# Kernel tuning notes

Measured on AMD Instinct MI355X. Metric: run time of the kernel, lower is better.

Reference implementation:

```python
import jax, jax.numpy as jnp
import numpy as np

B, N, M = 4, 8192, 8192

def setup_inputs() -> dict:
    key = jax.random.key(0)
    k1, k2 = jax.random.split(key)
    xyz1 = jax.random.normal(k1, (B, N, 3), dtype=jnp.float32)
    xyz2 = jax.random.normal(k2, (B, M, 3), dtype=jnp.float32)
    return {"xyz1": xyz1, "xyz2": xyz2}

def reference(xyz1, xyz2):
    sq1 = jnp.sum(xyz1 * xyz1, axis=-1)                      # [B,N]
    sq2 = jnp.sum(xyz2 * xyz2, axis=-1)                      # [B,M]
    inner = jnp.einsum('bnd,bmd->bnm', xyz1, xyz2)           # [B,N,M]
    d = sq1[:, :, None] + sq2[:, None, :] - 2.0 * inner      # squared dists
    dist1 = jnp.min(d, axis=2)                               # [B,N] nearest in xyz2
    dist2 = jnp.min(d, axis=1)                               # [B,M] nearest in xyz1
    return (dist1, dist2)
```

## Files before the change

kernel.cpp:

```cpp
#include <hip/hip_runtime.h>


typedef short bf16x8 __attribute__((ext_vector_type(8)));
typedef float f32x16 __attribute__((ext_vector_type(16)));

constexpr int Bc  = 4;
constexpr int Nc  = 8192;
constexpr int NT  = Nc / 32;
constexpr int SEG = 8;
constexpr int TPS = NT / SEG;

__device__ inline unsigned short f2bf(float x) {
    unsigned u = __float_as_uint(x);
    unsigned r = (u + 0x7FFFu + ((u >> 16) & 1u)) >> 16;
    return (unsigned short)r;
}
__device__ inline float bf2f(unsigned short h) {
    return __uint_as_float(((unsigned)h) << 16);
}
__device__ inline unsigned pack2(unsigned short lo, unsigned short hi) {
    return (unsigned)lo | ((unsigned)hi << 16);
}

__global__ void init_out_inf(float* __restrict__ out, int n) {
    int i = blockIdx.x * blockDim.x + threadIdx.x;
    int stride = gridDim.x * blockDim.x;
    for (; i < n; i += stride) out[i] = __uint_as_float(0x7F800000u);
}

__global__ void pack_both(const float* __restrict__ xyz1,
                          const float* __restrict__ xyz2,
                          uint4* __restrict__ qf, uint4* __restrict__ tf) {
    const int tid   = blockIdx.x * 256 + threadIdx.x;
    const int cloud = blockIdx.y;
    const float* src = cloud ? xyz2 : xyz1;
    const int lane = tid & 63;
    const int tile = (tid >> 6) & (NT - 1);
    const int b    = tid >> 14;
    const int pt   = tile * 32 + (lane & 31);
    const int kg   = lane >> 5;
    const float* p = src + ((size_t)b * Nc + pt) * 3;
    float x = p[0], y = p[1], z = p[2];
    float sq = x * x + y * y + z * z;
    unsigned short xh = f2bf(x), yh = f2bf(y), zh = f2bf(z);
    unsigned short xl = f2bf(x - bf2f(xh)), yl = f2bf(y - bf2f(yh)), zl = f2bf(z - bf2f(zh));
    unsigned short sh = f2bf(sq), sl = f2bf(sq - bf2f(sh));
    unsigned short m2xh = f2bf(-2.0f * bf2f(xh));
    unsigned short m2yh = f2bf(-2.0f * bf2f(yh));
    unsigned short m2zh = f2bf(-2.0f * bf2f(zh));
    unsigned short m2xl = f2bf(-2.0f * (x - bf2f(xh)));
    unsigned short m2yl = f2bf(-2.0f * (y - bf2f(yh)));
    unsigned short m2zl = f2bf(-2.0f * (z - bf2f(zh)));
    const unsigned short ONE = 0x3F80;
    uint4 q, t;
    if (kg == 0) {
        q.x = pack2(xh, xh); q.y = pack2(xl, yh);
        q.z = pack2(yh, yl); q.w = pack2(zh, zh);
        t.x = pack2(m2xh, m2xl); t.y = pack2(m2xh, m2yh);
        t.z = pack2(m2yl, m2yh); t.w = pack2(m2zh, m2zl);
    } else {
        q.x = pack2(zl, sh); q.y = pack2(sl, ONE);
        q.z = pack2(ONE, 0); q.w = 0;
        t.x = pack2(m2zh, ONE); t.y = pack2(ONE, sh);
        t.z = pack2(sl, 0);     t.w = 0;
    }
    const size_t FR = (size_t)Bc * NT * 64;
    qf[(size_t)cloud * FR + tid] = q;
    tf[(size_t)cloud * FR + tid] = t;
}

__global__ __launch_bounds__(256) void chamfer_dir(
    const uint4* __restrict__ qf,
    const uint4* __restrict__ tf,
    float* __restrict__ out) {
    __shared__ float sRed[4][32][33];
    const int tid = threadIdx.x, lane = tid & 63, wave = tid >> 6;
    const int z = blockIdx.z, dir = z >> 2, b = z & 3, seg = blockIdx.y;
    const int qc = dir, tc = dir ^ 1;
    const size_t FR = (size_t)Bc * NT * 64;

    const int n_tile = blockIdx.x * 4 + wave;
    const bf16x8 av = __builtin_bit_cast(bf16x8,
        qf[(size_t)qc * FR + ((size_t)(b * NT + n_tile)) * 64 + lane]);
    f32x16 zc{};
    float rmin[16];
    #pragma unroll
    for (int r = 0; r < 16; ++r) rmin[r] = INFINITY;

    const uint4* bp = tf + (size_t)tc * FR + ((size_t)(b * NT + seg * TPS)) * 64 + lane;
    #pragma unroll 4
    for (int mt = 0; mt < TPS; ++mt) {
        const bf16x8 bv = __builtin_bit_cast(bf16x8, bp[(size_t)mt * 64]);
        const f32x16 d = __builtin_amdgcn_mfma_f32_32x32x16_bf16(av, bv, zc, 0, 0, 0);
        #pragma unroll
        for (int r = 0; r < 16; ++r) rmin[r] = fminf(rmin[r], d[r]);
    }

    const int col = lane & 31, hi = lane >> 5;
    #pragma unroll
    for (int r = 0; r < 16; ++r) {
        const int row = (r & 3) + 8 * (r >> 2) + 4 * hi;
        sRed[wave][row][col] = rmin[r];
    }
    __syncthreads();

    const int row2 = tid >> 1, half = tid & 1;
    const int w = row2 >> 5, rr = row2 & 31;
    const float* rp = &sRed[w][rr][half * 16];
    float v0 = fminf(fminf(rp[0], rp[1]),  fminf(rp[2], rp[3]));
    float v1 = fminf(fminf(rp[4], rp[5]),  fminf(rp[6], rp[7]));
    float v2 = fminf(fminf(rp[8], rp[9]),  fminf(rp[10], rp[11]));
    float v3 = fminf(fminf(rp[12], rp[13]), fminf(rp[14], rp[15]));
    float v = fminf(fminf(v0, v1), fminf(v2, v3));
    v = fminf(v, __shfl_xor(v, 1));
    if (!half) {
        const int n = (blockIdx.x * 4 + w) * 32 + rr;
        unsigned* o = (unsigned*)out + (size_t)dir * Bc * Nc + (size_t)b * Nc + n;
        atomicMin(o, __float_as_uint(fmaxf(v, 0.0f)));
    }
}

constexpr int QPT = 2, TPB = 256;
__global__ void pack_pts(const float* __restrict__ src, float4* __restrict__ dst, int npts) {
    int i = blockIdx.x * blockDim.x + threadIdx.x;
    if (i < npts) {
        float x = src[3 * i], y = src[3 * i + 1], z = src[3 * i + 2];
        dst[i] = make_float4(x, y, z, x * x + y * y + z * z);
    }
}
__global__ __launch_bounds__(TPB, 8) void chamfer_fb(
    const float* __restrict__ xyz1, const float* __restrict__ xyz2,
    const float4* __restrict__ p1, const float4* __restrict__ p2,
    float* __restrict__ out) {
    const int z = blockIdx.z, dir = z >> 2, b = z & 3, seg = blockIdx.y;
    const float*  qry  = dir ? xyz2 : xyz1;
    const float4* tgt4 = dir ? p1 : p2;
    float* o = out + (size_t)dir * Bc * Nc + (size_t)b * Nc;
    const int q0 = blockIdx.x * (TPB * QPT) + threadIdx.x;
    float m2x[QPT], m2y[QPT], m2z[QPT], qsq[QPT];
    #pragma unroll
    for (int j = 0; j < QPT; ++j) {
        const float* qp = qry + ((size_t)b * Nc + q0 + j * TPB) * 3;
        float x = qp[0], y = qp[1], zz = qp[2];
        m2x[j] = -2.f * x; m2y[j] = -2.f * y; m2z[j] = -2.f * zz;
        qsq[j] = x * x + y * y + zz * zz;
    }
    constexpr int seg_pts = Nc / 16;
    const float4* t = tgt4 + (size_t)b * Nc + (size_t)seg * seg_pts;
    float mn0[QPT], mn1[QPT];
    #pragma unroll
    for (int j = 0; j < QPT; ++j) { mn0[j] = INFINITY; mn1[j] = INFINITY; }
    #pragma unroll 4
    for (int i = 0; i < seg_pts; i += 2) {
        const float4 t0 = t[i], t1 = t[i + 1];
        #pragma unroll
        for (int j = 0; j < QPT; ++j) {
            mn0[j] = fminf(mn0[j], fmaf(m2x[j], t0.x, fmaf(m2y[j], t0.y, fmaf(m2z[j], t0.z, t0.w))));
            mn1[j] = fminf(mn1[j], fmaf(m2x[j], t1.x, fmaf(m2y[j], t1.y, fmaf(m2z[j], t1.z, t1.w))));
        }
    }
    #pragma unroll
    for (int j = 0; j < QPT; ++j) {
        float d = fmaxf(qsq[j] + fminf(mn0[j], mn1[j]), 0.f);
        atomicMin((unsigned*)(o + q0 + j * TPB), __float_as_uint(d));
    }
}

extern "C" void kernel_launch(void* const* d_in, const int* in_sizes, int n_in,
                              void* d_out, int out_size, void* d_ws, size_t ws_size,
                              hipStream_t stream) {
    const float* xyz1 = (const float*)d_in[0];
    const float* xyz2 = (const float*)d_in[1];
    float* out = (float*)d_out;

    const size_t FR = (size_t)Bc * NT * 64;
    const size_t need = 4 * FR * sizeof(uint4);

    init_out_inf<<<dim3(64), dim3(256), 0, stream>>>(out, out_size);

    if (ws_size >= need) {
        uint4* qf = (uint4*)d_ws;
        uint4* tf = qf + 2 * FR;
        pack_both<<<dim3(FR / 256, 2), dim3(256), 0, stream>>>(xyz1, xyz2, qf, tf);
        dim3 grid(NT / 4, SEG, 2 * Bc);
        chamfer_dir<<<grid, dim3(256), 0, stream>>>(qf, tf, out);
    } else if (ws_size >= 2 * (size_t)Bc * Nc * sizeof(float4)) {
        float4* p1 = (float4*)d_ws;
        float4* p2 = p1 + Bc * Nc;
        pack_pts<<<dim3(Bc * Nc / 256), dim3(256), 0, stream>>>(xyz1, p1, Bc * Nc);
        pack_pts<<<dim3(Bc * Nc / 256), dim3(256), 0, stream>>>(xyz2, p2, Bc * Nc);
        dim3 grid(Nc / (TPB * QPT), 16, 2 * Bc);
        chamfer_fb<<<grid, dim3(TPB), 0, stream>>>(xyz1, xyz2, p1, p2, out);
    }
}
```

Measured before the change: 45.02 us.

## Register-block four query tiles per wave and prefetch target fragments

Each wave now holds four query tiles in registers and reuses every loaded target fragment across four MFMAs, which cuts target-fragment loads per MFMA and shrinks the grid fourfold. The next target fragment is prefetched in software while the current one is used. The LDS-based row reduction and barrier are replaced by wave-level xor-shuffle reductions followed by per-row atomicMin from lane 0 of each half-wave. The cost is higher register pressure from 64 running minima per lane and fewer blocks, which may lower occupancy.

Measured after the change: 56.06 us. 24.5% more time.

```diff
diff --git a/kernel.cpp b/kernel.cpp
--- a/kernel.cpp
+++ b/kernel.cpp
@@ -9,6 +9,7 @@
 constexpr int NT  = Nc / 32;
 constexpr int SEG = 8;
 constexpr int TPS = NT / SEG;
+constexpr int QT  = 4;
 
 __device__ inline unsigned short f2bf(float x) {
     unsigned u = __float_as_uint(x);
@@ -69,54 +70,62 @@
     tf[(size_t)cloud * FR + tid] = t;
 }
 
-__global__ __launch_bounds__(256) void chamfer_dir(
+__global__ __launch_bounds__(256) void chamfer_rb(
     const uint4* __restrict__ qf,
     const uint4* __restrict__ tf,
     float* __restrict__ out) {
-    __shared__ float sRed[4][32][33];
     const int tid = threadIdx.x, lane = tid & 63, wave = tid >> 6;
     const int z = blockIdx.z, dir = z >> 2, b = z & 3, seg = blockIdx.y;
     const int qc = dir, tc = dir ^ 1;
     const size_t FR = (size_t)Bc * NT * 64;
 
-    const int n_tile = blockIdx.x * 4 + wave;
-    const bf16x8 av = __builtin_bit_cast(bf16x8,
-        qf[(size_t)qc * FR + ((size_t)(b * NT + n_tile)) * 64 + lane]);
+    const int tile0 = blockIdx.x * (4 * QT) + wave * QT;
+    bf16x8 av[QT];
+    #pragma unroll
+    for (int qt = 0; qt < QT; ++qt)
+        av[qt] = __builtin_bit_cast(bf16x8,
+            qf[(size_t)qc * FR + ((size_t)(b * NT + tile0 + qt)) * 64 + lane]);
+
     f32x16 zc{};
-    float rmin[16];
-    #pragma unroll
-    for (int r = 0; r < 16; ++r) rmin[r] = INFINITY;
+    float rmin[QT][16];
+    #pragma unroll
+    for (int qt = 0; qt < QT; ++qt)
+        #pragma unroll
+        for (int r = 0; r < 16; ++r) rmin[qt][r] = INFINITY;
 
     const uint4* bp = tf + (size_t)tc * FR + ((size_t)(b * NT + seg * TPS)) * 64 + lane;
-    #pragma unroll 4
+    bf16x8 bv = __builtin_bit_cast(bf16x8, bp[0]);
+    #pragma unroll 2
     for (int mt = 0; mt < TPS; ++mt) {
-        const bf16x8 bv = __builtin_bit_cast(bf16x8, bp[(size_t)mt * 64]);
-        const f32x16 d = __builtin_amdgcn_mfma_f32_32x32x16_bf16(av, bv, zc, 0, 0, 0);
-        #pragma unroll
-        for (int r = 0; r < 16; ++r) rmin[r] = fminf(rmin[r], d[r]);
-    }
-
-    const int col = lane & 31, hi = lane >> 5;
-    #pragma unroll
-    for (int r = 0; r < 16; ++r) {
-        const int row = (r & 3) + 8 * (r >> 2) + 4 * hi;
-        sRed[wave][row][col] = rmin[r];
-    }
-    __syncthreads();
-
-    const int row2 = tid >> 1, half = tid & 1;
-    const int w = row2 >> 5, rr = row2 & 31;
-    const float* rp = &sRed[w][rr][half * 16];
-    float v0 = fminf(fminf(rp[0], rp[1]),  fminf(rp[2], rp[3]));
-    float v1 = fminf(fminf(rp[4], rp[5]),  fminf(rp[6], rp[7]));
-    float v2 = fminf(fminf(rp[8], rp[9]),  fminf(rp[10], rp[11]));
-    float v3 = fminf(fminf(rp[12], rp[13]), fminf(rp[14], rp[15]));
-    float v = fminf(fminf(v0, v1), fminf(v2, v3));
-    v = fminf(v, __shfl_xor(v, 1));
-    if (!half) {
-        const int n = (blockIdx.x * 4 + w) * 32 + rr;
-        unsigned* o = (unsigned*)out + (size_t)dir * Bc * Nc + (size_t)b * Nc + n;
-        atomicMin(o, __float_as_uint(fmaxf(v, 0.0f)));
+        bf16x8 nbv = bv;
+        if (mt + 1 < TPS)
+            nbv = __builtin_bit_cast(bf16x8, bp[(size_t)(mt + 1) * 64]);
+        #pragma unroll
+        for (int qt = 0; qt < QT; ++qt) {
+            const f32x16 d = __builtin_amdgcn_mfma_f32_32x32x16_bf16(av[qt], bv, zc, 0, 0, 0);
+            #pragma unroll
+            for (int r = 0; r < 16; ++r) rmin[qt][r] = fminf(rmin[qt][r], d[r]);
+        }
+        bv = nbv;
+    }
+
+    const int hi = lane >> 5;
+    #pragma unroll
+    for (int qt = 0; qt < QT; ++qt) {
+        #pragma unroll
+        for (int m = 1; m <= 16; m <<= 1)
+            #pragma unroll
+            for (int r = 0; r < 16; ++r)
+                rmin[qt][r] = fminf(rmin[qt][r], __shfl_xor(rmin[qt][r], m));
+        if ((lane & 31) == 0) {
+            unsigned* d1 = (unsigned*)out + (size_t)dir * Bc * Nc + (size_t)b * Nc
+                         + (size_t)(tile0 + qt) * 32;
+            #pragma unroll
+            for (int r = 0; r < 16; ++r) {
+                const int row = (r & 3) + 8 * (r >> 2) + 4 * hi;
+                atomicMin(&d1[row], __float_as_uint(fmaxf(rmin[qt][r], 0.0f)));
+            }
+        }
     }
 }
 
@@ -182,8 +191,8 @@
         uint4* qf = (uint4*)d_ws;
         uint4* tf = qf + 2 * FR;
         pack_both<<<dim3(FR / 256, 2), dim3(256), 0, stream>>>(xyz1, xyz2, qf, tf);
-        dim3 grid(NT / 4, SEG, 2 * Bc);
-        chamfer_dir<<<grid, dim3(256), 0, stream>>>(qf, tf, out);
+        dim3 grid(NT / (4 * QT), SEG, 2 * Bc);
+        chamfer_rb<<<grid, dim3(256), 0, stream>>>(qf, tf, out);
     } else if (ws_size >= 2 * (size_t)Bc * Nc * sizeof(float4)) {
         float4* p1 = (float4*)d_ws;
         float4* p2 = p1 + Bc * Nc;
```

## Stage target tiles in LDS, widen blocks to 8 waves, shuffle-reduce row minima

Applied to the files above, without the earlier changes.

Each block now copies its whole segment of packed target fragments (32 KB) into shared memory once, and 8 query waves read from there instead of each wave streaming the fragments from global memory. The main loop is unrolled to issue two MFMAs per step and merge their minima. The final reduction of each row over the 32 columns now uses cross-lane xor shuffles and per-lane atomics instead of a shared-memory transpose. This is meant to cut global/L2 traffic and the reduction barrier, at the cost of more LDS per block, an upfront load-then-barrier phase, and many shuffle instructions.

Result: slower. 53.58 us (+19.0%).

```diff
diff --git a/kernel.cpp b/kernel.cpp
--- a/kernel.cpp
+++ b/kernel.cpp
@@ -9,6 +9,7 @@
 constexpr int NT  = Nc / 32;
 constexpr int SEG = 8;
 constexpr int TPS = NT / SEG;
+constexpr int WPB = 8;
 
 __device__ inline unsigned short f2bf(float x) {
     unsigned u = __float_as_uint(x);
@@ -69,17 +70,22 @@
     tf[(size_t)cloud * FR + tid] = t;
 }
 
-__global__ __launch_bounds__(256) void chamfer_dir(
+__global__ __launch_bounds__(512, 6) void chamfer_lds(
     const uint4* __restrict__ qf,
     const uint4* __restrict__ tf,
     float* __restrict__ out) {
-    __shared__ float sRed[4][32][33];
+    __shared__ uint4 sB[TPS * 64];
     const int tid = threadIdx.x, lane = tid & 63, wave = tid >> 6;
     const int z = blockIdx.z, dir = z >> 2, b = z & 3, seg = blockIdx.y;
     const int qc = dir, tc = dir ^ 1;
     const size_t FR = (size_t)Bc * NT * 64;
 
-    const int n_tile = blockIdx.x * 4 + wave;
+    const uint4* bseg = tf + (size_t)tc * FR + ((size_t)(b * NT + seg * TPS)) * 64;
+    #pragma unroll
+    for (int i = 0; i < TPS * 64 / 512; ++i)
+        sB[tid + i * 512] = bseg[tid + i * 512];
+
+    const int n_tile = blockIdx.x * WPB + wave;
     const bf16x8 av = __builtin_bit_cast(bf16x8,
         qf[(size_t)qc * FR + ((size_t)(b * NT + n_tile)) * 64 + lane]);
     f32x16 zc{};
@@ -87,36 +93,33 @@
     #pragma unroll
     for (int r = 0; r < 16; ++r) rmin[r] = INFINITY;
 
-    const uint4* bp = tf + (size_t)tc * FR + ((size_t)(b * NT + seg * TPS)) * 64 + lane;
-    #pragma unroll 4
-    for (int mt = 0; mt < TPS; ++mt) {
-        const bf16x8 bv = __builtin_bit_cast(bf16x8, bp[(size_t)mt * 64]);
-        const f32x16 d = __builtin_amdgcn_mfma_f32_32x32x16_bf16(av, bv, zc, 0, 0, 0);
+    __syncthreads();
+
+    #pragma unroll 2
+    for (int mt = 0; mt < TPS; mt += 2) {
+        const bf16x8 bv0 = __builtin_bit_cast(bf16x8, sB[mt * 64 + lane]);
+        const bf16x8 bv1 = __builtin_bit_cast(bf16x8, sB[mt * 64 + 64 + lane]);
+        const f32x16 d0 = __builtin_amdgcn_mfma_f32_32x32x16_bf16(av, bv0, zc, 0, 0, 0);
+        const f32x16 d1 = __builtin_amdgcn_mfma_f32_32x32x16_bf16(av, bv1, zc, 0, 0, 0);
         #pragma unroll
-        for (int r = 0; r < 16; ++r) rmin[r] = fminf(rmin[r], d[r]);
+        for (int r = 0; r < 16; ++r)
+            rmin[r] = fminf(rmin[r], fminf(d0[r], d1[r]));
     }
 
-    const int col = lane & 31, hi = lane >> 5;
     #pragma unroll
-    for (int r = 0; r < 16; ++r) {
-        const int row = (r & 3) + 8 * (r >> 2) + 4 * hi;
-        sRed[wave][row][col] = rmin[r];
-    }
-    __syncthreads();
-
-    const int row2 = tid >> 1, half = tid & 1;
-    const int w = row2 >> 5, rr = row2 & 31;
-    const float* rp = &sRed[w][rr][half * 16];
-    float v0 = fminf(fminf(rp[0], rp[1]),  fminf(rp[2], rp[3]));
-    float v1 = fminf(fminf(rp[4], rp[5]),  fminf(rp[6], rp[7]));
-    float v2 = fminf(fminf(rp[8], rp[9]),  fminf(rp[10], rp[11]));
-    float v3 = fminf(fminf(rp[12], rp[13]), fminf(rp[14], rp[15]));
-    float v = fminf(fminf(v0, v1), fminf(v2, v3));
-    v = fminf(v, __shfl_xor(v, 1));
-    if (!half) {
-        const int n = (blockIdx.x * 4 + w) * 32 + rr;
-        unsigned* o = (unsigned*)out + (size_t)dir * Bc * Nc + (size_t)b * Nc + n;
-        atomicMin(o, __float_as_uint(fmaxf(v, 0.0f)));
+    for (int m = 1; m <= 16; m <<= 1)
+        #pragma unroll
+        for (int r = 0; r < 16; ++r)
+            rmin[r] = fminf(rmin[r], __shfl_xor(rmin[r], m));
+    if ((lane & 31) == 0) {
+        const int hi = lane >> 5;
+        unsigned* d1p = (unsigned*)out + (size_t)dir * Bc * Nc + (size_t)b * Nc
+                      + (size_t)n_tile * 32;
+        #pragma unroll
+        for (int r = 0; r < 16; ++r) {
+            const int row = (r & 3) + 8 * (r >> 2) + 4 * hi;
+            atomicMin(&d1p[row], __float_as_uint(fmaxf(rmin[r], 0.0f)));
+        }
     }
 }
 
@@ -182,8 +185,8 @@
         uint4* qf = (uint4*)d_ws;
         uint4* tf = qf + 2 * FR;
         pack_both<<<dim3(FR / 256, 2), dim3(256), 0, stream>>>(xyz1, xyz2, qf, tf);
-        dim3 grid(NT / 4, SEG, 2 * Bc);
-        chamfer_dir<<<grid, dim3(256), 0, stream>>>(qf, tf, out);
+        dim3 grid(NT / WPB, SEG, 2 * Bc);
+        chamfer_lds<<<grid, dim3(512), 0, stream>>>(qf, tf, out);
     } else if (ws_size >= 2 * (size_t)Bc * Nc * sizeof(float4)) {
         float4* p1 = (float4*)d_ws;
         float4* p2 = p1 + Bc * Nc;
```
